# Kernel tuning notes

Hardware: AMD Instinct MI355X
Metric: run time of the kernel (lower is better)

## Reference

```python
import jax, jax.numpy as jnp
import numpy as np

N, E, G = 50000, 800000, 64   # nodes, edges, graphs in batch
H, C = 4, 64                  # GAT heads, per-head channels (concat=False -> averaged)
F_IN, D_OUT = 16, 32
NEG_SLOPE = 0.2


def setup_inputs():
    key = jax.random.key(0)
    ks = jax.random.split(key, 20)
    s = 0.05
    inp = {
        "x": jax.random.normal(ks[0], (N, F_IN), jnp.float32),
        "edge_index": jax.random.randint(ks[1], (2, E), 0, N, dtype=jnp.int32),
        "batch": jnp.sort(jax.random.randint(ks[2], (N,), 0, G, dtype=jnp.int32)),
        "Wp": jax.random.normal(ks[3], (F_IN, H * C // H), jnp.float32) * s,  # 16 -> 64
        "bp": jnp.zeros((64,), jnp.float32),
        "Wo": jax.random.normal(ks[4], (64, D_OUT), jnp.float32) * s,
        "bo": jnp.zeros((D_OUT,), jnp.float32),
    }
    for l in range(3):
        inp[f"W{l}"] = jax.random.normal(ks[5 + 3 * l], (64, H * C), jnp.float32) * s
        inp[f"as{l}"] = jax.random.normal(ks[6 + 3 * l], (H, C), jnp.float32) * s
        inp[f"ad{l}"] = jax.random.normal(ks[7 + 3 * l], (H, C), jnp.float32) * s
        inp[f"b{l}"] = jnp.zeros((C,), jnp.float32)
    return inp


def _gat_layer(h, src, dst, W, a_src, a_dst, b):
    # h: [N, 64] -> per-head features [N, H, C]
    hw = (h @ W).reshape(N, H, C)
    # per-node attention logits [N, H]
    al_s = jnp.sum(hw * a_src, axis=-1)
    al_d = jnp.sum(hw * a_dst, axis=-1)
    # per-edge logits (src contributes alpha_src, dst contributes alpha_dst)
    e = jax.nn.leaky_relu(al_s[src] + al_d[dst], NEG_SLOPE)  # [Et, H]
    # neighbor-wise softmax over edges grouped by destination node
    emax = jax.ops.segment_max(e, dst, num_segments=N)
    ex = jnp.exp(e - emax[dst])
    denom = jax.ops.segment_sum(ex, dst, num_segments=N)
    alpha = ex / denom[dst]                                   # [Et, H]
    # weighted scatter-add of source features to destinations
    msg = alpha[:, :, None] * hw[src]                         # [Et, H, C]
    out = jax.ops.segment_sum(msg, dst, num_segments=N)       # [N, H, C]
    return out.mean(axis=1) + b                               # concat=False: head mean


def reference(x, edge_index, batch, Wp, bp, W0, as0, ad0, b0,
              W1, as1, ad1, b1, W2, as2, ad2, b2, Wo, bo):
    # add self-loops once (PyG GATConv default add_self_loops=True)
    loop = jnp.arange(N, dtype=edge_index.dtype)
    src = jnp.concatenate([edge_index[0], loop])
    dst = jnp.concatenate([edge_index[1], loop])

    h = jax.nn.relu(x @ Wp + bp)
    for (W, a_s, a_d, b) in ((W0, as0, ad0, b0), (W1, as1, ad1, b1), (W2, as2, ad2, b2)):
        h = jax.nn.relu(_gat_layer(h, src, dst, W, a_s, a_d, b))

    # global mean pool over graphs
    sums = jax.ops.segment_sum(h, batch, num_segments=G)
    cnt = jax.ops.segment_sum(jnp.ones((N,), h.dtype), batch, num_segments=G)
    pooled = sums / jnp.maximum(cnt, 1.0)[:, None]
    return pooled @ Wo + bo
```

## Files before the change

### kernel.cpp

```cpp
#include <hip/hip_runtime.h>

#define NEG_SLOPE 0.2f

typedef __attribute__((ext_vector_type(8))) short bf16x8;
typedef __attribute__((ext_vector_type(8))) unsigned short u16x8;
typedef __attribute__((ext_vector_type(4))) float f32x4;

__device__ __forceinline__ float lrelu(float x) { return fmaxf(x, NEG_SLOPE * x); }

__device__ __forceinline__ float bf2f(unsigned short u) {
  return __uint_as_float(((unsigned int)u) << 16);
}
__device__ __forceinline__ unsigned short f2bf(float f) {
  unsigned int u = __float_as_uint(f);
  u += 0x7fffu + ((u >> 16) & 1u);
  return (unsigned short)(u >> 16);
}

__global__ void proj_kernel(const float* __restrict__ x, const float* __restrict__ Wp,
                            const float* __restrict__ bp, unsigned short* __restrict__ h,
                            int n_nodes) {
  int idx = blockIdx.x * blockDim.x + threadIdx.x;
  int n = idx >> 6, c = idx & 63;
  if (n >= n_nodes) return;
  float acc = bp[c];
#pragma unroll
  for (int k = 0; k < 16; ++k) acc += x[n * 16 + k] * Wp[k * 64 + c];
  h[n * 64 + c] = f2bf(fmaxf(acc, 0.f));
}

__global__ void hist_kernel(const int* __restrict__ dst, int* __restrict__ deg, int e) {
  int i = blockIdx.x * blockDim.x + threadIdx.x;
  if (i < e) atomicAdd(&deg[dst[i]], 1);
}

__global__ __launch_bounds__(256) void scan_a(const int* __restrict__ deg, int* __restrict__ rowp,
                                              int* __restrict__ bsum, int n) {
  __shared__ int s[256];
  int t = threadIdx.x;
  int base = blockIdx.x * 1024 + t * 4;
  int d0 = (base + 0 < n) ? deg[base + 0] + 1 : 0;
  int d1 = (base + 1 < n) ? deg[base + 1] + 1 : 0;
  int d2 = (base + 2 < n) ? deg[base + 2] + 1 : 0;
  int d3 = (base + 3 < n) ? deg[base + 3] + 1 : 0;
  s[t] = d0 + d1 + d2 + d3;
  __syncthreads();
  for (int off = 1; off < 256; off <<= 1) {
    int v = 0;
    if (t >= off) v = s[t - off];
    __syncthreads();
    if (t >= off) s[t] += v;
    __syncthreads();
  }
  int p = (t == 0) ? 0 : s[t - 1];
  if (base + 0 < n) rowp[base + 0] = p;
  p += d0;
  if (base + 1 < n) rowp[base + 1] = p;
  p += d1;
  if (base + 2 < n) rowp[base + 2] = p;
  p += d2;
  if (base + 3 < n) rowp[base + 3] = p;
  if (t == 255) bsum[blockIdx.x] = s[255];
}

__global__ void scan_b(const int* __restrict__ bsum, int* __restrict__ bpre, int nb) {
  int t = threadIdx.x;
  int v = (t < nb) ? bsum[t] : 0;
  int orig = v;
#pragma unroll
  for (int off = 1; off < 64; off <<= 1) {
    int u = __shfl_up(v, off);
    if (t >= off) v += u;
  }
  bpre[t] = v - orig;
  if (t == 63) bpre[64] = v;
}

__global__ void scan_c(int* __restrict__ rowp, const int* __restrict__ bpre,
                       int* __restrict__ cnt, int* __restrict__ col, int n) {
  int i = blockIdx.x * blockDim.x + threadIdx.x;
  if (i < n) {
    int r = rowp[i] + bpre[i >> 10];
    rowp[i] = r;
    cnt[i] = 1;
    col[r] = i;
  }
  if (i == 0) rowp[n] = bpre[64];
}

__global__ void scatter_kernel(const int* __restrict__ src, const int* __restrict__ dst,
                               const int* __restrict__ rowp, int* __restrict__ cnt,
                               int* __restrict__ col, int e) {
  int i = blockIdx.x * blockDim.x + threadIdx.x;
  if (i < e) {
    int d = dst[i];
    int pos = rowp[d] + atomicAdd(&cnt[d], 1);
    col[pos] = src[i];
  }
}

__global__ __launch_bounds__(256) void prep_kernel(
    const float* __restrict__ W0, const float* __restrict__ as0, const float* __restrict__ ad0,
    const float* __restrict__ W1, const float* __restrict__ as1, const float* __restrict__ ad1,
    const float* __restrict__ W2, const float* __restrict__ as2, const float* __restrict__ ad2,
    unsigned short* __restrict__ Wsw, unsigned short* __restrict__ Wasw) {
  __shared__ float wa[512];
  int l = blockIdx.x;
  const float* W  = l == 0 ? W0  : l == 1 ? W1  : W2;
  const float* as = l == 0 ? as0 : l == 1 ? as1 : as2;
  const float* ad = l == 0 ? ad0 : l == 1 ? ad1 : ad2;
  int t = threadIdx.x;
  {
    int k = t >> 2, h = t & 3;
    float ss = 0.f, sd = 0.f;
    for (int c = 0; c < 64; ++c) {
      float w = W[k * 256 + h * 64 + c];
      ss += w * as[h * 64 + c];
      sd += w * ad[h * 64 + c];
    }
    wa[k * 8 + h] = ss;
    wa[k * 8 + 4 + h] = sd;
  }
  __syncthreads();
  for (int s = t; s < 2048; s += 256) {
    int nt = s >> 7, kk = (s >> 6) & 1, lane = s & 63;
    int kq = lane >> 4, r = lane & 15;
#pragma unroll
    for (int j = 0; j < 8; ++j) {
      int k = kk * 32 + kq * 8 + j;
      Wsw[(size_t)l * 16384 + (size_t)s * 8 + j] = f2bf(W[k * 256 + nt * 16 + r]);
    }
  }
  if (t < 128) {
    int lane = t & 63, kq = lane >> 4, r = lane & 15;
    int kk = t >> 6;
#pragma unroll
    for (int j = 0; j < 8; ++j) {
      int k = kk * 32 + kq * 8 + j;
      float v = (r < 8) ? wa[k * 8 + r] : 0.f;
      Wasw[l * 1024 + t * 8 + j] = f2bf(v);
    }
  }
}

__global__ __launch_bounds__(256) void hw_kernel(const unsigned short* __restrict__ hb,
                                                 const unsigned short* __restrict__ Wsw,
                                                 const unsigned short* __restrict__ Wasw,
                                                 unsigned short* __restrict__ hwb,
                                                 float* __restrict__ al_s, float* __restrict__ al_d,
                                                 int n_nodes) {
  __shared__ unsigned short st[64][264];
  int t = threadIdx.x;
  int w = t >> 6, lane = t & 63;
  int kq = lane >> 4, r16 = lane & 15;
  int n0 = blockIdx.x << 6;

  bf16x8 a[4][2];
#pragma unroll
  for (int m = 0; m < 4; ++m) {
    int row = min(n0 + m * 16 + r16, n_nodes - 1);
    const unsigned short* p = hb + (size_t)row * 64 + kq * 8;
    a[m][0] = *(const bf16x8*)(p);
    a[m][1] = *(const bf16x8*)(p + 32);
  }
  bf16x8 b[4][2];
#pragma unroll
  for (int nt = 0; nt < 4; ++nt) {
    int ntg = w * 4 + nt;
    const unsigned short* p = Wsw + ((size_t)ntg * 128 + lane) * 8;
    b[nt][0] = *(const bf16x8*)(p);
    b[nt][1] = *(const bf16x8*)(p + 512);
  }

  f32x4 acc[4][4];
#pragma unroll
  for (int m = 0; m < 4; ++m)
#pragma unroll
    for (int nt = 0; nt < 4; ++nt) acc[m][nt] = (f32x4){0.f, 0.f, 0.f, 0.f};

#pragma unroll
  for (int m = 0; m < 4; ++m)
#pragma unroll
    for (int nt = 0; nt < 4; ++nt) {
      acc[m][nt] = __builtin_amdgcn_mfma_f32_16x16x32_bf16(a[m][0], b[nt][0], acc[m][nt], 0, 0, 0);
      acc[m][nt] = __builtin_amdgcn_mfma_f32_16x16x32_bf16(a[m][1], b[nt][1], acc[m][nt], 0, 0, 0);
    }

#pragma unroll
  for (int m = 0; m < 4; ++m)
#pragma unroll
    for (int j = 0; j < 4; ++j) {
      int row = m * 16 + kq * 4 + j;
#pragma unroll
      for (int nt = 0; nt < 4; ++nt)
        st[row][(w * 4 + nt) * 16 + r16] = f2bf(acc[m][nt][j]);
    }
  __syncthreads();

  int rmax = min(64, n_nodes - n0);
  for (int i = t; i < (rmax << 5); i += 256) {
    int row = i >> 5, ch = i & 31;
    *(u16x8*)(hwb + (size_t)(n0 + row) * 256 + ch * 8) = *(const u16x8*)(&st[row][ch * 8]);
  }

  bf16x8 ba0 = *(const bf16x8*)(Wasw + lane * 8);
  bf16x8 ba1 = *(const bf16x8*)(Wasw + (64 + lane) * 8);
  f32x4 accl = (f32x4){0.f, 0.f, 0.f, 0.f};
  accl = __builtin_amdgcn_mfma_f32_16x16x32_bf16(a[w][0], ba0, accl, 0, 0, 0);
  accl = __builtin_amdgcn_mfma_f32_16x16x32_bf16(a[w][1], ba1, accl, 0, 0, 0);
  if (r16 < 8) {
#pragma unroll
    for (int j = 0; j < 4; ++j) {
      int row = n0 + w * 16 + kq * 4 + j;
      if (row < n_nodes) {
        if (r16 < 4) al_s[row * 4 + r16] = accl[j];
        else         al_d[row * 4 + (r16 - 4)] = accl[j];
      }
    }
  }
}

__global__ __launch_bounds__(256) void gat_agg(const int* __restrict__ rowp, const int* __restrict__ col,
                                               const float* __restrict__ alS, const float* __restrict__ alD,
                                               const unsigned short* __restrict__ hwb,
                                               const float* __restrict__ bias,
                                               unsigned short* __restrict__ hout,
                                               int n_nodes) {
  __shared__ uint2 pw[4][64 * 4];
  int t = threadIdx.x;
  int wslot = t >> 6, lane = t & 63;
  int node = blockIdx.x * 4 + wslot;
  if (node >= n_nodes) return;
  int base = rowp[node];
  int degv = rowp[node + 1] - base;
  int l31 = lane & 31;
  int half = lane >> 5;
  int headw = l31 >> 3;
  unsigned int laneoff = (unsigned int)l31 << 4;
  float4 ald4 = *(const float4*)(alD + (size_t)node * 4);

  float a0 = 0.f, a1 = 0.f, a2 = 0.f, a3 = 0.f;
  float a4 = 0.f, a5 = 0.f, a6 = 0.f, a7 = 0.f, denom = 0.f;

  for (int c0 = 0; c0 < degv; c0 += 64) {
    int cnt = min(64, degv - c0);
    {
      unsigned int ab = 0u;
      float w0 = 0.f, w1 = 0.f, w2 = 0.f, w3 = 0.f;
      if (lane < cnt) {
        int s = col[base + c0 + lane];
        float4 as4 = *(const float4*)(alS + (size_t)s * 4);
        ab = (unsigned int)s << 9;
        w0 = __expf(lrelu(as4.x + ald4.x));
        w1 = __expf(lrelu(as4.y + ald4.y));
        w2 = __expf(lrelu(as4.z + ald4.z));
        w3 = __expf(lrelu(as4.w + ald4.w));
      }
      uint4* pd = (uint4*)&pw[wslot][lane * 4];
      pd[0] = make_uint4(ab, __float_as_uint(w0), ab, __float_as_uint(w1));
      pd[1] = make_uint4(ab, __float_as_uint(w2), ab, __float_as_uint(w3));
    }
    int iters = (cnt + 1) >> 1;
#pragma unroll 4
    for (int i = 0; i < iters; ++i) {
      int e = i * 2 + half;
      uint2 p = pw[wslot][e * 4 + headw];
      float w = __uint_as_float(p.y);
      uint4 v = *(const uint4*)((const char*)hwb + (p.x + laneoff));
      denom += w;
      a0 += w * __uint_as_float(v.x << 16);
      a1 += w * __uint_as_float(v.x & 0xffff0000u);
      a2 += w * __uint_as_float(v.y << 16);
      a3 += w * __uint_as_float(v.y & 0xffff0000u);
      a4 += w * __uint_as_float(v.z << 16);
      a5 += w * __uint_as_float(v.z & 0xffff0000u);
      a6 += w * __uint_as_float(v.w << 16);
      a7 += w * __uint_as_float(v.w & 0xffff0000u);
    }
  }

  denom += __shfl_xor(denom, 32);
  a0 += __shfl_xor(a0, 32); a1 += __shfl_xor(a1, 32);
  a2 += __shfl_xor(a2, 32); a3 += __shfl_xor(a3, 32);
  a4 += __shfl_xor(a4, 32); a5 += __shfl_xor(a5, 32);
  a6 += __shfl_xor(a6, 32); a7 += __shfl_xor(a7, 32);
  float inv = 1.f / denom;
  a0 *= inv; a1 *= inv; a2 *= inv; a3 *= inv;
  a4 *= inv; a5 *= inv; a6 *= inv; a7 *= inv;

  a0 += __shfl_xor(a0, 8); a0 += __shfl_xor(a0, 16);
  a1 += __shfl_xor(a1, 8); a1 += __shfl_xor(a1, 16);
  a2 += __shfl_xor(a2, 8); a2 += __shfl_xor(a2, 16);
  a3 += __shfl_xor(a3, 8); a3 += __shfl_xor(a3, 16);
  a4 += __shfl_xor(a4, 8); a4 += __shfl_xor(a4, 16);
  a5 += __shfl_xor(a5, 8); a5 += __shfl_xor(a5, 16);
  a6 += __shfl_xor(a6, 8); a6 += __shfl_xor(a6, 16);
  a7 += __shfl_xor(a7, 8); a7 += __shfl_xor(a7, 16);

  if (lane < 8) {
    const float* bp = bias + lane * 8;
    float4 b0 = *(const float4*)(bp);
    float4 b1 = *(const float4*)(bp + 4);
    ushort4 o0, o1;
    o0.x = f2bf(fmaxf(0.25f * a0 + b0.x, 0.f));
    o0.y = f2bf(fmaxf(0.25f * a1 + b0.y, 0.f));
    o0.z = f2bf(fmaxf(0.25f * a2 + b0.z, 0.f));
    o0.w = f2bf(fmaxf(0.25f * a3 + b0.w, 0.f));
    o1.x = f2bf(fmaxf(0.25f * a4 + b1.x, 0.f));
    o1.y = f2bf(fmaxf(0.25f * a5 + b1.y, 0.f));
    o1.z = f2bf(fmaxf(0.25f * a6 + b1.z, 0.f));
    o1.w = f2bf(fmaxf(0.25f * a7 + b1.w, 0.f));
    unsigned short* op = hout + (size_t)node * 64 + lane * 8;
    *(ushort4*)(op) = o0;
    *(ushort4*)(op + 4) = o1;
  }
}

__global__ void pool_kernel(const unsigned short* __restrict__ h, const int* __restrict__ batch,
                            float* __restrict__ pool, float* __restrict__ pcnt, int n_nodes) {
  int c = threadIdx.x;
  int n0 = blockIdx.x * 64;
  int n1 = min(n0 + 64, n_nodes);
  float acc = 0.f;
  int run = 0;
  int gcur = batch[n0];
  for (int n = n0; n < n1; ++n) {
    int g = batch[n];
    if (g != gcur) {
      atomicAdd(&pool[gcur * 64 + c], acc);
      if (c == 0) atomicAdd(&pcnt[gcur], (float)run);
      acc = 0.f; run = 0; gcur = g;
    }
    acc += bf2f(h[(size_t)n * 64 + c]);
    ++run;
  }
  atomicAdd(&pool[gcur * 64 + c], acc);
  if (c == 0) atomicAdd(&pcnt[gcur], (float)run);
}

__global__ void out_kernel(const float* __restrict__ pool, const float* __restrict__ pcnt,
                           const float* __restrict__ Wo, const float* __restrict__ bo,
                           float* __restrict__ out, int g_total) {
  int idx = blockIdx.x * blockDim.x + threadIdx.x;
  if (idx >= g_total * 32) return;
  int g = idx >> 5, d = idx & 31;
  float inv = 1.f / fmaxf(pcnt[g], 1.f);
  float acc = bo[d];
#pragma unroll
  for (int c = 0; c < 64; ++c) acc += (pool[g * 64 + c] * inv) * Wo[c * 32 + d];
  out[idx] = acc;
}

extern "C" void kernel_launch(void* const* d_in, const int* in_sizes, int n_in,
                              void* d_out, int out_size, void* d_ws, size_t ws_size,
                              hipStream_t stream) {
  const float* x     = (const float*)d_in[0];
  const int*   ei    = (const int*)d_in[1];
  const int*   batch = (const int*)d_in[2];
  const float* Wp    = (const float*)d_in[3];
  const float* bp    = (const float*)d_in[4];
  const float* Wo    = (const float*)d_in[5];
  const float* bo    = (const float*)d_in[6];
  const float* Wl[3]  = {(const float*)d_in[7],  (const float*)d_in[11], (const float*)d_in[15]};
  const float* Asl[3] = {(const float*)d_in[8],  (const float*)d_in[12], (const float*)d_in[16]};
  const float* Adl[3] = {(const float*)d_in[9],  (const float*)d_in[13], (const float*)d_in[17]};
  const float* Bl[3]  = {(const float*)d_in[10], (const float*)d_in[14], (const float*)d_in[18]};

  const int N = in_sizes[0] / 16;
  const int E = in_sizes[1] / 2;
  const int G = out_size / 32;
  const int Et = E + N;
  const int* src = ei;
  const int* dst = ei + E;
  const int NB = (N + 1023) / 1024;

  char* ws = (char*)d_ws;
  size_t off = 0;
  auto take = [&](size_t bytes) -> void* {
    void* p = ws + off;
    off = (off + bytes + 255) & ~(size_t)255;
    return p;
  };
  unsigned short* h_a = (unsigned short*)take((size_t)N * 64 * 2);
  unsigned short* h_b = (unsigned short*)take((size_t)N * 64 * 2);
  unsigned short* hwb = (unsigned short*)take((size_t)N * 256 * 2);
  float* alS   = (float*)take((size_t)N * 4 * 4);
  float* alD   = (float*)take((size_t)N * 4 * 4);
  int*   deg   = (int*)take((size_t)N * 4);
  int*   cnt   = (int*)take((size_t)N * 4);
  int*   rowp  = (int*)take((size_t)(N + 1) * 4);
  int*   col   = (int*)take((size_t)Et * 4);
  int*   bsum  = (int*)take((size_t)64 * 4);
  int*   bpre  = (int*)take((size_t)65 * 4);
  unsigned short* Wsw  = (unsigned short*)take((size_t)3 * 16384 * 2);
  unsigned short* Wasw = (unsigned short*)take((size_t)3 * 1024 * 2);
  float* pool  = (float*)take((size_t)G * 64 * 4);
  float* pcnt  = (float*)take((size_t)G * 4);
  (void)ws_size; (void)n_in;

  prep_kernel<<<3, 256, 0, stream>>>(Wl[0], Asl[0], Adl[0], Wl[1], Asl[1], Adl[1],
                                     Wl[2], Asl[2], Adl[2], Wsw, Wasw);

  hipMemsetAsync(deg, 0, (size_t)N * 4, stream);
  hist_kernel<<<(E + 255) / 256, 256, 0, stream>>>(dst, deg, E);
  scan_a<<<NB, 256, 0, stream>>>(deg, rowp, bsum, N);
  scan_b<<<1, 64, 0, stream>>>(bsum, bpre, NB);
  scan_c<<<(N + 255) / 256, 256, 0, stream>>>(rowp, bpre, cnt, col, N);
  scatter_kernel<<<(E + 255) / 256, 256, 0, stream>>>(src, dst, rowp, cnt, col, E);

  proj_kernel<<<((size_t)N * 64 + 255) / 256, 256, 0, stream>>>(x, Wp, bp, h_a, N);

  const unsigned short* hin = h_a;
  unsigned short* hout = h_b;
  for (int l = 0; l < 3; ++l) {
    hw_kernel<<<(N + 63) / 64, 256, 0, stream>>>(hin, Wsw + (size_t)l * 16384,
                                                 Wasw + (size_t)l * 1024, hwb, alS, alD, N);
    gat_agg<<<(N + 3) / 4, 256, 0, stream>>>(rowp, col, alS, alD, hwb, Bl[l], hout, N);
    const unsigned short* tmp = hout;
    hout = (unsigned short*)hin;
    hin = tmp;
  }

  hipMemsetAsync(pool, 0, (size_t)((char*)(pcnt + G) - (char*)pool), stream);
  pool_kernel<<<(N + 63) / 64, 64, 0, stream>>>(hin, batch, pool, pcnt, N);
  out_kernel<<<(G * 32 + 255) / 256, 256, 0, stream>>>(pool, pcnt, Wo, bo, (float*)d_out, G);
}
```

Before: 410.5 us.

## Fuse projection into first GAT matmul, merge pooling with output, vectorize CSR build

The input projection moves into the first hw_kernel through a FIRST template path that computes relu(x@Wp+bp) into shared memory. Pooling and the output linear layer become one per-graph kernel that finds each graph's node range by binary search over the sorted batch, which removes the atomics and the memsets. Zeroing of the degree array moves into extra blocks of prep_kernel. The histogram and scatter kernels now process four edges per thread using int4 loads. Together these cut kernel launches and memsets, at the cost of a serialized per-graph reduction and an extra barrier in hw_kernel.

Result: slower. 432.4 us (+5.3%).

```diff
diff --git a/kernel.cpp b/kernel.cpp
--- a/kernel.cpp
+++ b/kernel.cpp
@@ -17,21 +17,17 @@
   return (unsigned short)(u >> 16);
 }
 
-__global__ void proj_kernel(const float* __restrict__ x, const float* __restrict__ Wp,
-                            const float* __restrict__ bp, unsigned short* __restrict__ h,
-                            int n_nodes) {
-  int idx = blockIdx.x * blockDim.x + threadIdx.x;
-  int n = idx >> 6, c = idx & 63;
-  if (n >= n_nodes) return;
-  float acc = bp[c];
-#pragma unroll
-  for (int k = 0; k < 16; ++k) acc += x[n * 16 + k] * Wp[k * 64 + c];
-  h[n * 64 + c] = f2bf(fmaxf(acc, 0.f));
-}
-
 __global__ void hist_kernel(const int* __restrict__ dst, int* __restrict__ deg, int e) {
-  int i = blockIdx.x * blockDim.x + threadIdx.x;
-  if (i < e) atomicAdd(&deg[dst[i]], 1);
+  int i4 = (blockIdx.x * blockDim.x + threadIdx.x) * 4;
+  if (i4 + 4 <= e) {
+    int4 d = *(const int4*)(dst + i4);
+    atomicAdd(&deg[d.x], 1);
+    atomicAdd(&deg[d.y], 1);
+    atomicAdd(&deg[d.z], 1);
+    atomicAdd(&deg[d.w], 1);
+  } else {
+    for (int j = i4; j < e; ++j) atomicAdd(&deg[dst[j]], 1);
+  }
 }
 
 __global__ __launch_bounds__(256) void scan_a(const int* __restrict__ deg, int* __restrict__ rowp,
@@ -91,11 +87,20 @@
 __global__ void scatter_kernel(const int* __restrict__ src, const int* __restrict__ dst,
                                const int* __restrict__ rowp, int* __restrict__ cnt,
                                int* __restrict__ col, int e) {
-  int i = blockIdx.x * blockDim.x + threadIdx.x;
-  if (i < e) {
-    int d = dst[i];
-    int pos = rowp[d] + atomicAdd(&cnt[d], 1);
-    col[pos] = src[i];
+  int i4 = (blockIdx.x * blockDim.x + threadIdx.x) * 4;
+  if (i4 >= e) return;
+  if (i4 + 4 <= e) {
+    int4 s4 = *(const int4*)(src + i4);
+    int4 d4 = *(const int4*)(dst + i4);
+    col[rowp[d4.x] + atomicAdd(&cnt[d4.x], 1)] = s4.x;
+    col[rowp[d4.y] + atomicAdd(&cnt[d4.y], 1)] = s4.y;
+    col[rowp[d4.z] + atomicAdd(&cnt[d4.z], 1)] = s4.z;
+    col[rowp[d4.w] + atomicAdd(&cnt[d4.w], 1)] = s4.w;
+  } else {
+    for (int j = i4; j < e; ++j) {
+      int d = dst[j];
+      col[rowp[d] + atomicAdd(&cnt[d], 1)] = src[j];
+    }
   }
 }
 
@@ -103,7 +108,14 @@
     const float* __restrict__ W0, const float* __restrict__ as0, const float* __restrict__ ad0,
     const float* __restrict__ W1, const float* __restrict__ as1, const float* __restrict__ ad1,
     const float* __restrict__ W2, const float* __restrict__ as2, const float* __restrict__ ad2,
-    unsigned short* __restrict__ Wsw, unsigned short* __restrict__ Wasw) {
+    unsigned short* __restrict__ Wsw, unsigned short* __restrict__ Wasw,
+    int* __restrict__ deg, int n_nodes) {
+  if (blockIdx.x >= 3) {
+    int i = ((blockIdx.x - 3) * 256 + threadIdx.x) * 4;
+    if (i + 4 <= n_nodes) *(int4*)(deg + i) = make_int4(0, 0, 0, 0);
+    else for (int j = i; j < n_nodes; ++j) deg[j] = 0;
+    return;
+  }
   __shared__ float wa[512];
   int l = blockIdx.x;
   const float* W  = l == 0 ? W0  : l == 1 ? W1  : W2;
@@ -143,25 +155,58 @@
   }
 }
 
+template <bool FIRST>
 __global__ __launch_bounds__(256) void hw_kernel(const unsigned short* __restrict__ hb,
+                                                 const float* __restrict__ x,
+                                                 const float* __restrict__ Wp,
+                                                 const float* __restrict__ bp,
                                                  const unsigned short* __restrict__ Wsw,
                                                  const unsigned short* __restrict__ Wasw,
                                                  unsigned short* __restrict__ hwb,
                                                  float* __restrict__ al_s, float* __restrict__ al_d,
                                                  int n_nodes) {
   __shared__ unsigned short st[64][264];
+  unsigned short (*hs)[72] = reinterpret_cast<unsigned short(*)[72]>(&st[0][0]);
   int t = threadIdx.x;
   int w = t >> 6, lane = t & 63;
   int kq = lane >> 4, r16 = lane & 15;
   int n0 = blockIdx.x << 6;
 
+  if constexpr (FIRST) {
+    __shared__ float wp_s[1024];
+    __shared__ float bp_s[64];
+    for (int i = t; i < 1024; i += 256) wp_s[i] = Wp[i];
+    if (t < 64) bp_s[t] = bp[t];
+    __syncthreads();
+#pragma unroll
+    for (int i = 0; i < 16; ++i) {
+      int r = i * 4 + w;
+      int row = n0 + r;
+      float acc = 0.f;
+      if (row < n_nodes) {
+        acc = bp_s[lane];
+        const float* xr = x + (size_t)row * 16;
+#pragma unroll
+        for (int k = 0; k < 16; ++k) acc += xr[k] * wp_s[k * 64 + lane];
+        acc = fmaxf(acc, 0.f);
+      }
+      hs[r][lane] = f2bf(acc);
+    }
+    __syncthreads();
+  }
+
   bf16x8 a[4][2];
 #pragma unroll
   for (int m = 0; m < 4; ++m) {
-    int row = min(n0 + m * 16 + r16, n_nodes - 1);
-    const unsigned short* p = hb + (size_t)row * 64 + kq * 8;
-    a[m][0] = *(const bf16x8*)(p);
-    a[m][1] = *(const bf16x8*)(p + 32);
+    if constexpr (FIRST) {
+      a[m][0] = *(const bf16x8*)&hs[m * 16 + r16][kq * 8];
+      a[m][1] = *(const bf16x8*)&hs[m * 16 + r16][kq * 8 + 32];
+    } else {
+      int row = min(n0 + m * 16 + r16, n_nodes - 1);
+      const unsigned short* p = hb + (size_t)row * 64 + kq * 8;
+      a[m][0] = *(const bf16x8*)(p);
+      a[m][1] = *(const bf16x8*)(p + 32);
+    }
   }
   bf16x8 b[4][2];
 #pragma unroll
@@ -186,6 +231,7 @@
       acc[m][nt] = __builtin_amdgcn_mfma_f32_16x16x32_bf16(a[m][1], b[nt][1], acc[m][nt], 0, 0, 0);
     }
 
+  __syncthreads();
 #pragma unroll
   for (int m = 0; m < 4; ++m)
 #pragma unroll
@@ -316,39 +362,37 @@
   }
 }
 
-__global__ void pool_kernel(const unsigned short* __restrict__ h, const int* __restrict__ batch,
-                            float* __restrict__ pool, float* __restrict__ pcnt, int n_nodes) {
-  int c = threadIdx.x;
-  int n0 = blockIdx.x * 64;
-  int n1 = min(n0 + 64, n_nodes);
+__global__ __launch_bounds__(256) void poolout_kernel(const unsigned short* __restrict__ h,
+                                                      const int* __restrict__ batch,
+                                                      const float* __restrict__ Wo,
+                                                      const float* __restrict__ bo,
+                                                      float* __restrict__ out, int n_nodes) {
+  int g = blockIdx.x;
+  int lo = 0, hi = n_nodes;
+  while (lo < hi) { int mid = (lo + hi) >> 1; if (batch[mid] < g) lo = mid + 1; else hi = mid; }
+  int s = lo;
+  hi = n_nodes;
+  while (lo < hi) { int mid = (lo + hi) >> 1; if (batch[mid] < g + 1) lo = mid + 1; else hi = mid; }
+  int e = lo;
+
+  int t = threadIdx.x, c = t & 63, wv = t >> 6;
   float acc = 0.f;
-  int run = 0;
-  int gcur = batch[n0];
-  for (int n = n0; n < n1; ++n) {
-    int g = batch[n];
-    if (g != gcur) {
-      atomicAdd(&pool[gcur * 64 + c], acc);
-      if (c == 0) atomicAdd(&pcnt[gcur], (float)run);
-      acc = 0.f; run = 0; gcur = g;
-    }
-    acc += bf2f(h[(size_t)n * 64 + c]);
-    ++run;
-  }
-  atomicAdd(&pool[gcur * 64 + c], acc);
-  if (c == 0) atomicAdd(&pcnt[gcur], (float)run);
-}
-
-__global__ void out_kernel(const float* __restrict__ pool, const float* __restrict__ pcnt,
-                           const float* __restrict__ Wo, const float* __restrict__ bo,
-                           float* __restrict__ out, int g_total) {
-  int idx = blockIdx.x * blockDim.x + threadIdx.x;
-  if (idx >= g_total * 32) return;
-  int g = idx >> 5, d = idx & 31;
-  float inv = 1.f / fmaxf(pcnt[g], 1.f);
-  float acc = bo[d];
-#pragma unroll
-  for (int c = 0; c < 64; ++c) acc += (pool[g * 64 + c] * inv) * Wo[c * 32 + d];
-  out[idx] = acc;
+  for (int r = s + wv; r < e; r += 4) acc += bf2f(h[(size_t)r * 64 + c]);
+  __shared__ float red[4][64];
+  __shared__ float pooled[64];
+  red[wv][c] = acc;
+  __syncthreads();
+  if (t < 64) {
+    float cntf = (float)max(e - s, 1);
+    pooled[t] = (red[0][t] + red[1][t] + red[2][t] + red[3][t]) / cntf;
+  }
+  __syncthreads();
+  if (t < 32) {
+    float a = bo[t];
+#pragma unroll 8
+    for (int k = 0; k < 64; ++k) a += pooled[k] * Wo[k * 32 + t];
+    out[g * 32 + t] = a;
+  }
 }
 
 extern "C" void kernel_launch(void* const* d_in, const int* in_sizes, int n_in,
@@ -394,34 +438,27 @@
   int*   bpre  = (int*)take((size_t)65 * 4);
   unsigned short* Wsw  = (unsigned short*)take((size_t)3 * 16384 * 2);
   unsigned short* Wasw = (unsigned short*)take((size_t)3 * 1024 * 2);
-  float* pool  = (float*)take((size_t)G * 64 * 4);
-  float* pcnt  = (float*)take((size_t)G * 4);
   (void)ws_size; (void)n_in;
 
-  prep_kernel<<<3, 256, 0, stream>>>(Wl[0], Asl[0], Adl[0], Wl[1], Asl[1], Adl[1],
-                                     Wl[2], Asl[2], Adl[2], Wsw, Wasw);
-
-  hipMemsetAsync(deg, 0, (size_t)N * 4, stream);
-  hist_kernel<<<(E + 255) / 256, 256, 0, stream>>>(dst, deg, E);
+  prep_kernel<<<3 + (N + 1023) / 1024, 256, 0, stream>>>(
+      Wl[0], Asl[0], Adl[0], Wl[1], Asl[1], Adl[1], Wl[2], Asl[2], Adl[2],
+      Wsw, Wasw, deg, N);
+
+  hist_kernel<<<(E / 4 + 255) / 256, 256, 0, stream>>>(dst, deg, E);
   scan_a<<<NB, 256, 0, stream>>>(deg, rowp, bsum, N);
   scan_b<<<1, 64, 0, stream>>>(bsum, bpre, NB);
   scan_c<<<(N + 255) / 256, 256, 0, stream>>>(rowp, bpre, cnt, col, N);
-  scatter_kernel<<<(E + 255) / 256, 256, 0, stream>>>(src, dst, rowp, cnt, col, E);
-
-  proj_kernel<<<((size_t)N * 64 + 255) / 256, 256, 0, stream>>>(x, Wp, bp, h_a, N);
-
-  const unsigned short* hin = h_a;
-  unsigned short* hout = h_b;
-  for (int l = 0; l < 3; ++l) {
-    hw_kernel<<<(N + 63) / 64, 256, 0, stream>>>(hin, Wsw + (size_t)l * 16384,
-                                                 Wasw + (size_t)l * 1024, hwb, alS, alD, N);
-    gat_agg<<<(N + 3) / 4, 256, 0, stream>>>(rowp, col, alS, alD, hwb, Bl[l], hout, N);
-    const unsigned short* tmp = hout;
-    hout = (unsigned short*)hin;
-    hin = tmp;
-  }
-
-  hipMemsetAsync(pool, 0, (size_t)((char*)(pcnt + G) - (char*)pool), stream);
-  pool_kernel<<<(N + 63) / 64, 64, 0, stream>>>(hin, batch, pool, pcnt, N);
-  out_kernel<<<(G * 32 + 255) / 256, 256, 0, stream>>>(pool, pcnt, Wo, bo, (float*)d_out, G);
-}
+  scatter_kernel<<<(E / 4 + 255) / 256, 256, 0, stream>>>(src, dst, rowp, cnt, col, E);
+
+  hw_kernel<true><<<(N + 63) / 64, 256, 0, stream>>>(nullptr, x, Wp, bp,
+                                                     Wsw, Wasw, hwb, alS, alD, N);
+  gat_agg<<<(N + 3) / 4, 256, 0, stream>>>(rowp, col, alS, alD, hwb, Bl[0], h_b, N);
+  hw_kernel<false><<<(N + 63) / 64, 256, 0, stream>>>(h_b, nullptr, nullptr, nullptr,
+                                                      Wsw + 16384, Wasw + 1024, hwb, alS, alD, N);
+  gat_agg<<<(N + 3) / 4, 256, 0, stream>>>(rowp, col, alS, alD, hwb, Bl[1], h_a, N);
+  hw_kernel<false><<<(N + 63) / 64, 256, 0, stream>>>(h_a, nullptr, nullptr, nullptr,
+                                                      Wsw + 32768, Wasw + 2048, hwb, alS, alD, N);
+  gat_agg<<<(N + 3) / 4, 256, 0, stream>>>(rowp, col, alS, alD, hwb, Bl[2], h_b, N);
+
+  poolout_kernel<<<G, 256, 0, stream>>>(h_b, batch, Wo, bo, (float*)d_out, N);
+}
```
